# Kernel tuning notes

Hardware: AMD Instinct MI355X
Metric: run time of the kernel (lower is better)

Reference implementation:

```python
import jax, jax.numpy as jnp
import numpy as np

B, N, V, H = 8, 2048, 256, 1024
EPS = 1e-5
NEG = -1e9


def _layernorm(x, g, b):
    m = jnp.mean(x, axis=-1, keepdims=True)
    v = jnp.mean((x - m) ** 2, axis=-1, keepdims=True)
    return (x - m) / jnp.sqrt(v + EPS) * g + b


def setup_inputs() -> dict:
    key = jax.random.key(0)
    ks = jax.random.split(key, 10)
    tril = jnp.tril(jnp.ones((N, N), jnp.float32))
    return {
        "h": jax.random.normal(ks[0], (B, N, V), jnp.float32),
        "mask_one": tril,                      # keep causal entries
        "mask_zero": NEG * (1.0 - tril),       # -inf-ish above diagonal
        "ln_attn_g": jnp.ones((V,), jnp.float32),
        "ln_attn_b": jnp.zeros((V,), jnp.float32),
        "ln_mlp_g": jnp.ones((V,), jnp.float32),
        "ln_mlp_b": jnp.zeros((V,), jnp.float32),
        "wv": jax.random.normal(ks[1], (V,), jnp.float32),
        "wv_bos": jax.random.normal(ks[2], (V,), jnp.float32),
        "wo_w": jax.random.normal(ks[3], (V, V), jnp.float32) / np.sqrt(V),
        "qk_bos": jax.random.normal(ks[4], (V,), jnp.float32),
        "qk_previous": jax.random.normal(ks[5], (V,), jnp.float32),
        "qk_direction": jnp.ones((V,), jnp.float32),  # middel_layer=False, frozen
        "w1": jax.random.normal(ks[6], (H, V), jnp.float32) / np.sqrt(V),
        "w2": jax.random.normal(ks[7], (V, H), jnp.float32) / np.sqrt(H),
    }


def reference(h, mask_one, mask_zero, ln_attn_g, ln_attn_b, ln_mlp_g, ln_mlp_b,
              wv, wv_bos, wo_w, qk_bos, qk_previous, qk_direction, w1, w2):
    b, n, v = h.shape
    # mask blends LayerNorm only into row 0 (BOS position)
    attn_input = h.at[:, 0, :].set(_layernorm(h[:, 0, :], ln_attn_g, ln_attn_b))
    # value states: diag(wv) on positions 1.., wo(wv_bos) at position 0
    values = attn_input[:, 1:, :] * wv                      # [B, N-1, V]
    v_bos = wo_w @ wv_bos                                   # Linear(bias=False)
    values = jnp.concatenate(
        [jnp.broadcast_to(v_bos, (b, 1, v)), values], axis=1)  # [B, N, V]
    # sparse QK logits: column 0 term + sub-diagonal term, densified then masked
    col0 = (attn_input @ qk_bos) * (attn_input[:, 0, :] @ qk_direction)[:, None]  # [B, N]
    d = attn_input @ qk_previous                            # [B, N]
    qk = jnp.zeros((b, n, n), h.dtype).at[:, :, 0].add(col0)
    idx = jnp.arange(1, n)
    qk = qk.at[:, idx, idx - 1].add(d[:, 1:])               # row r, col r-1 = d[:, r]
    qk = qk * mask_one + mask_zero
    attn_out = jax.nn.softmax(qk, axis=-1) @ values         # [B, N, V]
    # FFN branch with its own BOS-only LayerNorm blend
    mlp_input = h.at[:, 0, :].set(_layernorm(h[:, 0, :], ln_mlp_g, ln_mlp_b))
    mlp_out = jax.nn.relu(mlp_input @ w1.T) @ w2.T          # [B, N, V]
    return attn_out + mlp_out
```

## Files before the change

kernel.cpp:

```cpp
#include <hip/hip_runtime.h>
#include <hip/hip_bf16.h>

#define BB 8
#define NN 2048
#define VV 256
#define HH 1024
#define CHK 64
#define RPC 32
constexpr float EPS = 1e-5f;

typedef __attribute__((ext_vector_type(4))) float floatx4;
typedef __attribute__((ext_vector_type(8))) short short8;

__device__ __forceinline__ void load_lds16(const void* g, void* l) {
    __builtin_amdgcn_global_load_lds((const __attribute__((address_space(1))) void*)g,
                                     (__attribute__((address_space(3))) void*)l, 16, 0, 0);
}
__device__ __forceinline__ float bf16s_to_f(short s) {
    unsigned u = ((unsigned)(unsigned short)s) << 16;
    return __builtin_bit_cast(float, u);
}

__global__ __launch_bounds__(256) void scan_fused_kernel(
    const float* __restrict__ h,
    const float* __restrict__ g_attn, const float* __restrict__ b_attn,
    const float* __restrict__ g_mlp,  const float* __restrict__ b_mlp,
    const float* __restrict__ qk_dir,
    const float* __restrict__ wo_w,  const float* __restrict__ wv_bos,
    const float* __restrict__ wv,
    const float* __restrict__ qk_bos, const float* __restrict__ qk_prev,
    short* __restrict__ Xb,
    float* __restrict__ wpack,
    float* __restrict__ chunkSum,
    float* __restrict__ v_bos,
    const float* __restrict__ w1, const float* __restrict__ w2,
    short* __restrict__ w1b, short* __restrict__ w2b)
{
    __shared__ float lds[4][VV];
    __shared__ __align__(16) float mrow[VV];
    __shared__ float redA[4], redB[4], redC[4];
    int t = threadIdx.x;
    int wave = t >> 6, lane = t & 63;
    int b = blockIdx.x / CHK, c = blockIdx.x % CHK;

    float x0 = h[(size_t)b * NN * VV + t];
    float s = x0;
    for (int off = 32; off > 0; off >>= 1) s += __shfl_down(s, off);
    if (lane == 0) redA[wave] = s;
    __syncthreads();
    float m = (redA[0] + redA[1] + redA[2] + redA[3]) * (1.0f / VV);
    float xc = x0 - m;
    float sv = xc * xc;
    for (int off = 32; off > 0; off >>= 1) sv += __shfl_down(sv, off);
    if (lane == 0) redB[wave] = sv;
    __syncthreads();
    float var = (redB[0] + redB[1] + redB[2] + redB[3]) * (1.0f / VV);
    float inv = 1.0f / sqrtf(var + EPS);
    float an = xc * inv * g_attn[t] + b_attn[t];
    float mn = xc * inv * g_mlp[t]  + b_mlp[t];
    float sd = an * qk_dir[t];
    for (int off = 32; off > 0; off >>= 1) sd += __shfl_down(sd, off);
    if (lane == 0) redC[wave] = sd;
    mrow[t] = mn;
    __syncthreads();
    float s0b = redC[0] + redC[1] + redC[2] + redC[3];

    int r0 = c * RPC + wave * 8;
    float4 wv4 = reinterpret_cast<const float4*>(wv)[lane];
    float4 qb4 = reinterpret_cast<const float4*>(qk_bos)[lane];
    float4 qp4 = reinterpret_cast<const float4*>(qk_prev)[lane];
    float4 vsum = {0.f, 0.f, 0.f, 0.f};
#pragma unroll
    for (int rr = 0; rr < 8; ++rr) {
        int r = r0 + rr;
        size_t base = ((size_t)b * NN + r) * VV;
        float4 x = *reinterpret_cast<const float4*>(h + base + lane * 4);
        float4 xs = x;
        if (r == 0) xs = *reinterpret_cast<const float4*>(&mrow[lane * 4]);
        __hip_bfloat16 c0 = __float2bfloat16(xs.x), c1 = __float2bfloat16(xs.y),
                       c2 = __float2bfloat16(xs.z), c3 = __float2bfloat16(xs.w);
        short4 pk;
        pk.x = *reinterpret_cast<short*>(&c0);
        pk.y = *reinterpret_cast<short*>(&c1);
        pk.z = *reinterpret_cast<short*>(&c2);
        pk.w = *reinterpret_cast<short*>(&c3);
        *reinterpret_cast<short4*>(Xb + base + lane * 4) = pk;
        if (r != 0) {
            vsum.x += bf16s_to_f(pk.x) * wv4.x; vsum.y += bf16s_to_f(pk.y) * wv4.y;
            vsum.z += bf16s_to_f(pk.z) * wv4.z; vsum.w += bf16s_to_f(pk.w) * wv4.w;
        }
        float s1 = x.x * qb4.x + x.y * qb4.y + x.z * qb4.z + x.w * qb4.w;
        float s2 = x.x * qp4.x + x.y * qp4.y + x.z * qp4.z + x.w * qp4.w;
        for (int off = 32; off > 0; off >>= 1) {
            s1 += __shfl_down(s1, off);
            s2 += __shfl_down(s2, off);
        }
        if (lane == 0) {
            int gid = b * NN + r;
            float W0, WP, WZ;
            if (r == 0) { W0 = 1.f; WP = 0.f; WZ = 0.f; }
            else if (r == 1) {
                float a = s1 * s0b + s2;
                float mm = fmaxf(a, 0.f);
                float ea = expf(a - mm), ez = expf(-mm);
                float Z = ea + ez;
                W0 = ea / Z; WZ = ez / Z; WP = WZ;
            } else {
                float a = s1 * s0b;
                float mm = fmaxf(fmaxf(a, s2), 0.f);
                float ea = expf(a - mm), ed = expf(s2 - mm), ez = expf(-mm);
                float Z = ea + ed + (float)(r - 1) * ez;
                W0 = ea / Z; WP = ed / Z; WZ = ez / Z;
            }
            float4 wp4 = {W0, WP - WZ, WZ, 0.f};
            *reinterpret_cast<float4*>(wpack + (size_t)gid * 4) = wp4;
        }
    }
    reinterpret_cast<float4*>(lds[wave])[lane] = vsum;

    {
        int gi = blockIdx.x * 256 + threadIdx.x;
        size_t off = (size_t)gi * 4;
        const float* src; short* dst;
        if (off < (size_t)HH * VV) { src = w1 + off; dst = w1b + off; }
        else                       { src = w2 + (off - (size_t)HH * VV); dst = w2b + (off - (size_t)HH * VV); }
        float4 x = *reinterpret_cast<const float4*>(src);
        __hip_bfloat16 c0 = __float2bfloat16(x.x), c1 = __float2bfloat16(x.y),
                       c2 = __float2bfloat16(x.z), c3 = __float2bfloat16(x.w);
        short4 pk;
        pk.x = *reinterpret_cast<short*>(&c0);
        pk.y = *reinterpret_cast<short*>(&c1);
        pk.z = *reinterpret_cast<short*>(&c2);
        pk.w = *reinterpret_cast<short*>(&c3);
        *reinterpret_cast<short4*>(dst) = pk;
    }

    if (blockIdx.x == 0) {
        const float4* wp = reinterpret_cast<const float4*>(wo_w + (size_t)t * VV);
        const float4* vp = reinterpret_cast<const float4*>(wv_bos);
        float acc = 0.f;
        for (int j = 0; j < VV / 4; ++j) {
            float4 a = wp[j], bq = vp[j];
            acc += a.x * bq.x + a.y * bq.y + a.z * bq.z + a.w * bq.w;
        }
        v_bos[t] = acc;
    }

    __syncthreads();
    int v = threadIdx.x;
    chunkSum[((size_t)b * CHK + c) * VV + v] = lds[0][v] + lds[1][v] + lds[2][v] + lds[3][v];
}

__global__ __launch_bounds__(512) void mlp_fused5(const short* __restrict__ Xb,
                                                  const short* __restrict__ w1b,
                                                  const short* __restrict__ w2b,
                                                  const float* __restrict__ wv,
                                                  const float* __restrict__ v_bos,
                                                  const float* __restrict__ wpack,
                                                  const float* __restrict__ chunkSum,
                                                  float* __restrict__ out)
{
    __shared__ __align__(16) char smem[136 * 1024];
    short (*sW1)[64 * 256] = reinterpret_cast<short(*)[64 * 256]>(smem);
    short (*sW2)[256 * 64] = reinterpret_cast<short(*)[256 * 64]>(smem + 65536);
    short* sY = reinterpret_cast<short*>(smem + 131072);

    int wave = threadIdx.x >> 6, lane = threadIdx.x & 63;
    int wm = wave >> 2, wn = wave & 3;
    int ra = lane & 15, q = lane >> 4;
    int m0 = blockIdx.x * 64;
    int bq = m0 >> 11;
    int n0 = m0 & (NN - 1);

    auto stage = [&](int hc, int buf) {
#pragma unroll
        for (int it = 0; it < 4; ++it) {
            int g = wave * 4 + it;
            int n = g * 2 + (lane >> 5);
            int slot = lane & 31;
            load_lds16(w1b + (size_t)(hc * 64 + n) * VV + (slot ^ (n & 7)) * 8,
                       &sW1[buf][g * 512]);
        }
#pragma unroll
        for (int it = 0; it < 4; ++it) {
            int g = wave * 4 + it;
            int v = g * 8 + (lane >> 3);
            int slot = lane & 7;
            load_lds16(w2b + (size_t)v * HH + hc * 64 + (slot ^ (v & 7)) * 8,
                       &sW2[buf][g * 512]);
        }
    };

    stage(0, 0);

    short8 xf[8][2];
#pragma unroll
    for (int ks = 0; ks < 8; ++ks)
#pragma unroll
        for (int i = 0; i < 2; ++i)
            xf[ks][i] = *reinterpret_cast<const short8*>(
                Xb + (size_t)(m0 + wm * 32 + i * 16 + ra) * VV + ks * 32 + q * 8);

    int vcol = threadIdx.x & 255;
    int half = threadIdx.x >> 8;
    int cpre = (n0 >> 5) + half;
    float Sreg = 0.f;
    {
        const float* cs = chunkSum + (size_t)(bq * CHK) * VV + vcol;
#pragma unroll 4
        for (int c2 = 0; c2 < cpre; ++c2) Sreg += cs[(size_t)c2 * VV];
    }

    floatx4 oacc[2][4];
#pragma unroll
    for (int i = 0; i < 2; ++i)
#pragma unroll
        for (int j = 0; j < 4; ++j) oacc[i][j] = floatx4{0.f, 0.f, 0.f, 0.f};

    for (int hc = 0; hc < 16; ++hc) {
        int p = hc & 1;
        __syncthreads();
        if (hc < 15) stage(hc + 1, p ^ 1);

        floatx4 yacc[2];
        yacc[0] = floatx4{0.f, 0.f, 0.f, 0.f};
        yacc[1] = floatx4{0.f, 0.f, 0.f, 0.f};
        int nb = wn * 16 + ra;
#pragma unroll
        for (int ks = 0; ks < 8; ++ks) {
            short8 bfr = *reinterpret_cast<const short8*>(
                &sW1[p][nb * 256 + (((ks * 4 + q) ^ (ra & 7)) * 8)]);
#pragma unroll
            for (int i = 0; i < 2; ++i)
                yacc[i] = __builtin_amdgcn_mfma_f32_16x16x32_bf16(xf[ks][i], bfr, yacc[i], 0, 0, 0);
        }
#pragma unroll
        for (int i = 0; i < 2; ++i)
#pragma unroll
            for (int reg = 0; reg < 4; ++reg) {
                int mrow_ = wm * 32 + i * 16 + q * 4 + reg;
                int ke = wn * 16 + ra;
                __hip_bfloat16 hb = __float2bfloat16(fmaxf(yacc[i][reg], 0.f));
                sY[mrow_ * 64 + (((ke >> 3) ^ (mrow_ & 7)) * 8) + (ke & 7)] =
                    *reinterpret_cast<short*>(&hb);
            }
        __syncthreads();

#pragma unroll
        for (int kk = 0; kk < 2; ++kk) {
            short8 a2[2];
#pragma unroll
            for (int i = 0; i < 2; ++i) {
                int mrow_ = wm * 32 + i * 16 + ra;
                a2[i] = *reinterpret_cast<const short8*>(
                    &sY[mrow_ * 64 + (((kk * 4 + q) ^ (ra & 7)) * 8)]);
            }
#pragma unroll
            for (int j = 0; j < 4; ++j) {
                int v = wn * 64 + j * 16 + ra;
                short8 b2 = *reinterpret_cast<const short8*>(
                    &sW2[p][v * 64 + (((kk * 4 + q) ^ (ra & 7)) * 8)]);
#pragma unroll
                for (int i = 0; i < 2; ++i)
                    oacc[i][j] = __builtin_amdgcn_mfma_f32_16x16x32_bf16(a2[i], b2, oacc[i][j], 0, 0, 0);
            }
        }
    }

    __syncthreads();
    float* sOut = reinterpret_cast<float*>(smem);
#pragma unroll
    for (int i = 0; i < 2; ++i)
#pragma unroll
        for (int j = 0; j < 4; ++j)
#pragma unroll
            for (int reg = 0; reg < 4; ++reg) {
                int l = wm * 32 + i * 16 + q * 4 + reg;
                int col = wn * 64 + j * 16 + ra;
                sOut[l * 260 + col] = oacc[i][j][reg];
            }
    __syncthreads();

    {
        int r0 = n0 + half * RPC;
        float wvv = wv[vcol];
        float vb  = v_bos[vcol];
        float S = Sreg;
        float prev = 0.f;
        int r = r0;
        if (r0 == 0) {
            out[((size_t)bq * NN) * VV + vcol] = vb + sOut[0 * 260 + vcol];
            r = 1;
        } else {
            short p = Xb[((size_t)bq * NN + r0 - 1) * VV + vcol];
            prev = bf16s_to_f(p) * wvv;
        }
#pragma unroll 4
        for (; r < r0 + RPC; ++r) {
            size_t idx = ((size_t)bq * NN + r) * VV + vcol;
            float val = bf16s_to_f(Xb[idx]) * wvv;
            S += val;
            float4 wp4 = *reinterpret_cast<const float4*>(wpack + (size_t)(bq * NN + r) * 4);
            float o = wp4.x * vb + wp4.y * prev + wp4.z * S;
            prev = val;
            out[idx] = o + sOut[(r - n0) * 260 + vcol];
        }
    }
}

extern "C" void kernel_launch(void* const* d_in, const int* in_sizes, int n_in,
                              void* d_out, int out_size, void* d_ws, size_t ws_size,
                              hipStream_t stream)
{
    const float* h        = (const float*)d_in[0];
    const float* ln_attn_g = (const float*)d_in[3];
    const float* ln_attn_b = (const float*)d_in[4];
    const float* ln_mlp_g  = (const float*)d_in[5];
    const float* ln_mlp_b  = (const float*)d_in[6];
    const float* wv        = (const float*)d_in[7];
    const float* wv_bos    = (const float*)d_in[8];
    const float* wo_w      = (const float*)d_in[9];
    const float* qk_bos    = (const float*)d_in[10];
    const float* qk_prev   = (const float*)d_in[11];
    const float* qk_dir    = (const float*)d_in[12];
    const float* w1        = (const float*)d_in[13];
    const float* w2        = (const float*)d_in[14];
    float* out = (float*)d_out;

    float* v_bos     = (float*)d_ws;
    float* wpack     = v_bos + VV;
    float* chunkSum  = wpack + (size_t)BB * NN * 4;
    short* Xb        = (short*)(chunkSum + BB * CHK * VV);
    short* w1b       = (short*)(Xb + (size_t)BB * NN * VV);
    short* w2b       = w1b + HH * VV;

    scan_fused_kernel<<<BB * CHK, 256, 0, stream>>>(h, ln_attn_g, ln_attn_b,
                                                    ln_mlp_g, ln_mlp_b, qk_dir,
                                                    wo_w, wv_bos, wv, qk_bos, qk_prev,
                                                    Xb, wpack, chunkSum, v_bos,
                                                    w1, w2, w1b, w2b);
    mlp_fused5<<<256, 512, 0, stream>>>(Xb, w1b, w2b, wv, v_bos, wpack, chunkSum, out);
}
```

Measured before the change: 154.4 us.

## Fuse scan prep and MLP kernels into one cooperative kernel with grid sync

Merges the preprocessing kernel (bf16 conversion, softmax weights, chunk sums, weight casts, v_bos) and the MLP/scan kernel into a single cooperative launch of 256 blocks of 512 threads. A grid-wide barrier replaces the kernel boundary. Each block now preprocesses the same 64 rows it later consumes. This removes one launch and the gap between kernels. In exchange it depends on all 256 blocks with 136 KB of LDS each being co-resident, and it adds the cost of the grid sync.

```diff
diff --git a/kernel.cpp b/kernel.cpp
--- a/kernel.cpp
+++ b/kernel.cpp
@@ -1,5 +1,8 @@
 #include <hip/hip_runtime.h>
 #include <hip/hip_bf16.h>
+#include <hip/hip_cooperative_groups.h>
+
+namespace cg = cooperative_groups;
 
 #define BB 8
 #define NN 2048
@@ -21,7 +24,7 @@
     return __builtin_bit_cast(float, u);
 }
 
-__global__ __launch_bounds__(256) void scan_fused_kernel(
+__global__ __launch_bounds__(512) void fused_all(
     const float* __restrict__ h,
     const float* __restrict__ g_attn, const float* __restrict__ b_attn,
     const float* __restrict__ g_mlp,  const float* __restrict__ b_mlp,
@@ -29,97 +32,112 @@
     const float* __restrict__ wo_w,  const float* __restrict__ wv_bos,
     const float* __restrict__ wv,
     const float* __restrict__ qk_bos, const float* __restrict__ qk_prev,
+    const float* __restrict__ w1, const float* __restrict__ w2,
     short* __restrict__ Xb,
     float* __restrict__ wpack,
     float* __restrict__ chunkSum,
     float* __restrict__ v_bos,
-    const float* __restrict__ w1, const float* __restrict__ w2,
-    short* __restrict__ w1b, short* __restrict__ w2b)
+    short* __restrict__ w1b, short* __restrict__ w2b,
+    float* __restrict__ out)
 {
-    __shared__ float lds[4][VV];
-    __shared__ __align__(16) float mrow[VV];
-    __shared__ float redA[4], redB[4], redC[4];
-    int t = threadIdx.x;
-    int wave = t >> 6, lane = t & 63;
-    int b = blockIdx.x / CHK, c = blockIdx.x % CHK;
-
-    float x0 = h[(size_t)b * NN * VV + t];
+    __shared__ __align__(16) char smem[136 * 1024];
+    float (*lds8)[VV] = reinterpret_cast<float(*)[VV]>(smem);
+    float* mrow = reinterpret_cast<float*>(smem + 8 * VV * 4);
+    float* redA = mrow + VV;
+    float* redB = redA + 8;
+    float* redC = redB + 8;
+
+    int tid  = threadIdx.x;
+    int wave = tid >> 6, lane = tid & 63;
+    int half = tid >> 8;
+    int t256 = tid & 255;
+    int m0 = blockIdx.x * 64;
+    int b  = m0 >> 11;
+    int n0 = m0 & (NN - 1);
+
+    float x0 = h[(size_t)b * NN * VV + t256];
     float s = x0;
     for (int off = 32; off > 0; off >>= 1) s += __shfl_down(s, off);
     if (lane == 0) redA[wave] = s;
     __syncthreads();
-    float m = (redA[0] + redA[1] + redA[2] + redA[3]) * (1.0f / VV);
+    float m = (redA[half * 4 + 0] + redA[half * 4 + 1] +
+               redA[half * 4 + 2] + redA[half * 4 + 3]) * (1.0f / VV);
     float xc = x0 - m;
     float sv = xc * xc;
     for (int off = 32; off > 0; off >>= 1) sv += __shfl_down(sv, off);
     if (lane == 0) redB[wave] = sv;
     __syncthreads();
-    float var = (redB[0] + redB[1] + redB[2] + redB[3]) * (1.0f / VV);
+    float var = (redB[half * 4 + 0] + redB[half * 4 + 1] +
+                 redB[half * 4 + 2] + redB[half * 4 + 3]) * (1.0f / VV);
     float inv = 1.0f / sqrtf(var + EPS);
-    float an = xc * inv * g_attn[t] + b_attn[t];
-    float mn = xc * inv * g_mlp[t]  + b_mlp[t];
-    float sd = an * qk_dir[t];
+    float an = xc * inv * g_attn[t256] + b_attn[t256];
+    float mn = xc * inv * g_mlp[t256]  + b_mlp[t256];
+    float sd = an * qk_dir[t256];
     for (int off = 32; off > 0; off >>= 1) sd += __shfl_down(sd, off);
     if (lane == 0) redC[wave] = sd;
-    mrow[t] = mn;
-    __syncthreads();
-    float s0b = redC[0] + redC[1] + redC[2] + redC[3];
-
-    int r0 = c * RPC + wave * 8;
-    float4 wv4 = reinterpret_cast<const float4*>(wv)[lane];
-    float4 qb4 = reinterpret_cast<const float4*>(qk_bos)[lane];
-    float4 qp4 = reinterpret_cast<const float4*>(qk_prev)[lane];
-    float4 vsum = {0.f, 0.f, 0.f, 0.f};
-#pragma unroll
-    for (int rr = 0; rr < 8; ++rr) {
-        int r = r0 + rr;
-        size_t base = ((size_t)b * NN + r) * VV;
-        float4 x = *reinterpret_cast<const float4*>(h + base + lane * 4);
-        float4 xs = x;
-        if (r == 0) xs = *reinterpret_cast<const float4*>(&mrow[lane * 4]);
-        __hip_bfloat16 c0 = __float2bfloat16(xs.x), c1 = __float2bfloat16(xs.y),
-                       c2 = __float2bfloat16(xs.z), c3 = __float2bfloat16(xs.w);
-        short4 pk;
-        pk.x = *reinterpret_cast<short*>(&c0);
-        pk.y = *reinterpret_cast<short*>(&c1);
-        pk.z = *reinterpret_cast<short*>(&c2);
-        pk.w = *reinterpret_cast<short*>(&c3);
-        *reinterpret_cast<short4*>(Xb + base + lane * 4) = pk;
-        if (r != 0) {
-            vsum.x += bf16s_to_f(pk.x) * wv4.x; vsum.y += bf16s_to_f(pk.y) * wv4.y;
-            vsum.z += bf16s_to_f(pk.z) * wv4.z; vsum.w += bf16s_to_f(pk.w) * wv4.w;
-        }
-        float s1 = x.x * qb4.x + x.y * qb4.y + x.z * qb4.z + x.w * qb4.w;
-        float s2 = x.x * qp4.x + x.y * qp4.y + x.z * qp4.z + x.w * qp4.w;
-        for (int off = 32; off > 0; off >>= 1) {
-            s1 += __shfl_down(s1, off);
-            s2 += __shfl_down(s2, off);
-        }
-        if (lane == 0) {
-            int gid = b * NN + r;
-            float W0, WP, WZ;
-            if (r == 0) { W0 = 1.f; WP = 0.f; WZ = 0.f; }
-            else if (r == 1) {
-                float a = s1 * s0b + s2;
-                float mm = fmaxf(a, 0.f);
-                float ea = expf(a - mm), ez = expf(-mm);
-                float Z = ea + ez;
-                W0 = ea / Z; WZ = ez / Z; WP = WZ;
-            } else {
-                float a = s1 * s0b;
-                float mm = fmaxf(fmaxf(a, s2), 0.f);
-                float ea = expf(a - mm), ed = expf(s2 - mm), ez = expf(-mm);
-                float Z = ea + ed + (float)(r - 1) * ez;
-                W0 = ea / Z; WP = ed / Z; WZ = ez / Z;
-            }
-            float4 wp4 = {W0, WP - WZ, WZ, 0.f};
-            *reinterpret_cast<float4*>(wpack + (size_t)gid * 4) = wp4;
-        }
-    }
-    reinterpret_cast<float4*>(lds[wave])[lane] = vsum;
+    if (half == 0) mrow[t256] = mn;
+    __syncthreads();
+    float s0b = redC[half * 4 + 0] + redC[half * 4 + 1] +
+                redC[half * 4 + 2] + redC[half * 4 + 3];
 
     {
-        int gi = blockIdx.x * 256 + threadIdx.x;
+        int wave4 = wave & 3;
+        int r0 = n0 + half * RPC + wave4 * 8;
+        float4 wv4 = reinterpret_cast<const float4*>(wv)[lane];
+        float4 qb4 = reinterpret_cast<const float4*>(qk_bos)[lane];
+        float4 qp4 = reinterpret_cast<const float4*>(qk_prev)[lane];
+        float4 vsum = {0.f, 0.f, 0.f, 0.f};
+#pragma unroll
+        for (int rr = 0; rr < 8; ++rr) {
+            int r = r0 + rr;
+            size_t base = ((size_t)b * NN + r) * VV;
+            float4 x = *reinterpret_cast<const float4*>(h + base + lane * 4);
+            float4 xs = x;
+            if (r == 0) xs = *reinterpret_cast<const float4*>(&mrow[lane * 4]);
+            __hip_bfloat16 c0 = __float2bfloat16(xs.x), c1 = __float2bfloat16(xs.y),
+                           c2 = __float2bfloat16(xs.z), c3 = __float2bfloat16(xs.w);
+            short4 pk;
+            pk.x = *reinterpret_cast<short*>(&c0);
+            pk.y = *reinterpret_cast<short*>(&c1);
+            pk.z = *reinterpret_cast<short*>(&c2);
+            pk.w = *reinterpret_cast<short*>(&c3);
+            *reinterpret_cast<short4*>(Xb + base + lane * 4) = pk;
+            if (r != 0) {
+                vsum.x += bf16s_to_f(pk.x) * wv4.x; vsum.y += bf16s_to_f(pk.y) * wv4.y;
+                vsum.z += bf16s_to_f(pk.z) * wv4.z; vsum.w += bf16s_to_f(pk.w) * wv4.w;
+            }
+            float s1 = x.x * qb4.x + x.y * qb4.y + x.z * qb4.z + x.w * qb4.w;
+            float s2 = x.x * qp4.x + x.y * qp4.y + x.z * qp4.z + x.w * qp4.w;
+            for (int off = 32; off > 0; off >>= 1) {
+                s1 += __shfl_down(s1, off);
+                s2 += __shfl_down(s2, off);
+            }
+            if (lane == 0) {
+                int gid = b * NN + r;
+                float W0, WP, WZ;
+                if (r == 0) { W0 = 1.f; WP = 0.f; WZ = 0.f; }
+                else if (r == 1) {
+                    float a = s1 * s0b + s2;
+                    float mm = fmaxf(a, 0.f);
+                    float ea = expf(a - mm), ez = expf(-mm);
+                    float Z = ea + ez;
+                    W0 = ea / Z; WZ = ez / Z; WP = WZ;
+                } else {
+                    float a = s1 * s0b;
+                    float mm = fmaxf(fmaxf(a, s2), 0.f);
+                    float ea = expf(a - mm), ed = expf(s2 - mm), ez = expf(-mm);
+                    float Z = ea + ed + (float)(r - 1) * ez;
+                    W0 = ea / Z; WP = ed / Z; WZ = ez / Z;
+                }
+                float4 wp4 = {W0, WP - WZ, WZ, 0.f};
+                *reinterpret_cast<float4*>(wpack + (size_t)gid * 4) = wp4;
+            }
+        }
+        reinterpret_cast<float4*>(lds8[wave])[lane] = vsum;
+    }
+
+    {
+        int gi = blockIdx.x * 512 + tid;
         size_t off = (size_t)gi * 4;
         const float* src; short* dst;
         if (off < (size_t)HH * VV) { src = w1 + off; dst = w1b + off; }
@@ -135,42 +153,31 @@
         *reinterpret_cast<short4*>(dst) = pk;
     }
 
-    if (blockIdx.x == 0) {
-        const float4* wp = reinterpret_cast<const float4*>(wo_w + (size_t)t * VV);
+    if (blockIdx.x == 0 && tid < 256) {
+        const float4* wp = reinterpret_cast<const float4*>(wo_w + (size_t)tid * VV);
         const float4* vp = reinterpret_cast<const float4*>(wv_bos);
         float acc = 0.f;
         for (int j = 0; j < VV / 4; ++j) {
             float4 a = wp[j], bq = vp[j];
             acc += a.x * bq.x + a.y * bq.y + a.z * bq.z + a.w * bq.w;
         }
-        v_bos[t] = acc;
-    }
-
-    __syncthreads();
-    int v = threadIdx.x;
-    chunkSum[((size_t)b * CHK + c) * VV + v] = lds[0][v] + lds[1][v] + lds[2][v] + lds[3][v];
-}
-
-__global__ __launch_bounds__(512) void mlp_fused5(const short* __restrict__ Xb,
-                                                  const short* __restrict__ w1b,
-                                                  const short* __restrict__ w2b,
-                                                  const float* __restrict__ wv,
-                                                  const float* __restrict__ v_bos,
-                                                  const float* __restrict__ wpack,
-                                                  const float* __restrict__ chunkSum,
-                                                  float* __restrict__ out)
-{
-    __shared__ __align__(16) char smem[136 * 1024];
+        v_bos[tid] = acc;
+    }
+
+    __syncthreads();
+    chunkSum[((size_t)b * CHK + (n0 >> 5) + half) * VV + t256] =
+        lds8[half * 4 + 0][t256] + lds8[half * 4 + 1][t256] +
+        lds8[half * 4 + 2][t256] + lds8[half * 4 + 3][t256];
+
+    __threadfence();
+    cg::this_grid().sync();
+
     short (*sW1)[64 * 256] = reinterpret_cast<short(*)[64 * 256]>(smem);
     short (*sW2)[256 * 64] = reinterpret_cast<short(*)[256 * 64]>(smem + 65536);
     short* sY = reinterpret_cast<short*>(smem + 131072);
 
-    int wave = threadIdx.x >> 6, lane = threadIdx.x & 63;
     int wm = wave >> 2, wn = wave & 3;
     int ra = lane & 15, q = lane >> 4;
-    int m0 = blockIdx.x * 64;
-    int bq = m0 >> 11;
-    int n0 = m0 & (NN - 1);
 
     auto stage = [&](int hc, int buf) {
 #pragma unroll
@@ -201,12 +208,11 @@
             xf[ks][i] = *reinterpret_cast<const short8*>(
                 Xb + (size_t)(m0 + wm * 32 + i * 16 + ra) * VV + ks * 32 + q * 8);
 
-    int vcol = threadIdx.x & 255;
-    int half = threadIdx.x >> 8;
+    int vcol = t256;
     int cpre = (n0 >> 5) + half;
     float Sreg = 0.f;
     {
-        const float* cs = chunkSum + (size_t)(bq * CHK) * VV + vcol;
+        const float* cs = chunkSum + (size_t)(b * CHK) * VV + vcol;
 #pragma unroll 4
         for (int c2 = 0; c2 < cpre; ++c2) Sreg += cs[(size_t)c2 * VV];
     }
@@ -238,10 +244,10 @@
         for (int i = 0; i < 2; ++i)
 #pragma unroll
             for (int reg = 0; reg < 4; ++reg) {
-                int mrow_ = wm * 32 + i * 16 + q * 4 + reg;
+                int mr = wm * 32 + i * 16 + q * 4 + reg;
                 int ke = wn * 16 + ra;
                 __hip_bfloat16 hb = __float2bfloat16(fmaxf(yacc[i][reg], 0.f));
-                sY[mrow_ * 64 + (((ke >> 3) ^ (mrow_ & 7)) * 8) + (ke & 7)] =
+                sY[mr * 64 + (((ke >> 3) ^ (mr & 7)) * 8) + (ke & 7)] =
                     *reinterpret_cast<short*>(&hb);
             }
         __syncthreads();
@@ -251,9 +257,9 @@
             short8 a2[2];
 #pragma unroll
             for (int i = 0; i < 2; ++i) {
-                int mrow_ = wm * 32 + i * 16 + ra;
+                int mr = wm * 32 + i * 16 + ra;
                 a2[i] = *reinterpret_cast<const short8*>(
-                    &sY[mrow_ * 64 + (((kk * 4 + q) ^ (ra & 7)) * 8)]);
+                    &sY[mr * 64 + (((kk * 4 + q) ^ (ra & 7)) * 8)]);
             }
 #pragma unroll
             for (int j = 0; j < 4; ++j) {
@@ -289,18 +295,18 @@
         float prev = 0.f;
         int r = r0;
         if (r0 == 0) {
-            out[((size_t)bq * NN) * VV + vcol] = vb + sOut[0 * 260 + vcol];
+            out[((size_t)b * NN) * VV + vcol] = vb + sOut[0 * 260 + vcol];
             r = 1;
         } else {
-            short p = Xb[((size_t)bq * NN + r0 - 1) * VV + vcol];
-            prev = bf16s_to_f(p) * wvv;
+            short p2 = Xb[((size_t)b * NN + r0 - 1) * VV + vcol];
+            prev = bf16s_to_f(p2) * wvv;
         }
 #pragma unroll 4
         for (; r < r0 + RPC; ++r) {
-            size_t idx = ((size_t)bq * NN + r) * VV + vcol;
+            size_t idx = ((size_t)b * NN + r) * VV + vcol;
             float val = bf16s_to_f(Xb[idx]) * wvv;
             S += val;
-            float4 wp4 = *reinterpret_cast<const float4*>(wpack + (size_t)(bq * NN + r) * 4);
+            float4 wp4 = *reinterpret_cast<const float4*>(wpack + (size_t)(b * NN + r) * 4);
             float o = wp4.x * vb + wp4.y * prev + wp4.z * S;
             prev = val;
             out[idx] = o + sOut[(r - n0) * 260 + vcol];
@@ -334,10 +340,15 @@
     short* w1b       = (short*)(Xb + (size_t)BB * NN * VV);
     short* w2b       = w1b + HH * VV;
 
-    scan_fused_kernel<<<BB * CHK, 256, 0, stream>>>(h, ln_attn_g, ln_attn_b,
-                                                    ln_mlp_g, ln_mlp_b, qk_dir,
-                                                    wo_w, wv_bos, wv, qk_bos, qk_prev,
-                                                    Xb, wpack, chunkSum, v_bos,
-                                                    w1, w2, w1b, w2b);
-    mlp_fused5<<<256, 512, 0, stream>>>(Xb, w1b, w2b, wv, v_bos, wpack, chunkSum, out);
+    void* args[] = {
+        (void*)&h, (void*)&ln_attn_g, (void*)&ln_attn_b,
+        (void*)&ln_mlp_g, (void*)&ln_mlp_b, (void*)&qk_dir,
+        (void*)&wo_w, (void*)&wv_bos, (void*)&wv,
+        (void*)&qk_bos, (void*)&qk_prev,
+        (void*)&w1, (void*)&w2,
+        (void*)&Xb, (void*)&wpack, (void*)&chunkSum, (void*)&v_bos,
+        (void*)&w1b, (void*)&w2b, (void*)&out
+    };
+    hipLaunchCooperativeKernel((const void*)fused_all, dim3(256), dim3(512),
+                               args, 0, stream);
 }
```

New measurement: 262.0 us. 1.7x slower.
